# Performance work log

Measured on AMD Instinct MI355X. Metric: run time of the kernel, lower is better.

## Reference

```python
import jax, jax.numpy as jnp
import numpy as np

B, S, DIN, DOUT = 4, 2048, 4096, 4096
QMAX = 7  # int4 symmetric: values in [-8, 7]

def setup_inputs() -> dict:
    key = jax.random.key(0)
    kx, kq, ks, kb = jax.random.split(key, 4)
    x = jax.random.normal(kx, (B, S, DIN), dtype=jnp.float32)
    # int4 codes stored as int32, symmetric per-output-channel quantization
    qweight = jax.random.randint(kq, (DOUT, DIN), -8, 8, dtype=jnp.int32)
    # per-output-channel scale (max_abs / 7 style), strictly positive
    scale = jax.random.uniform(ks, (DOUT,), dtype=jnp.float32, minval=0.005, maxval=0.02)
    bias = jax.random.normal(kb, (DOUT,), dtype=jnp.float32)
    return {"x": x, "qweight": qweight, "scale": scale, "bias": bias}

def reference(x, qweight, scale, bias):
    # dequantize: per-output-channel scale broadcast over in_features
    weight = qweight.astype(jnp.float32) * scale[:, None]  # [DOUT, DIN]
    # F.linear: x @ weight.T + bias
    return jnp.einsum('bsi,oi->bso', x, weight) + bias
```

## Files before the change

### kernel.cpp

```cpp
#include <hip/hip_runtime.h>

typedef unsigned short u16;
typedef unsigned int u32;
typedef unsigned char u8;

typedef int i32x4 __attribute__((ext_vector_type(4)));

#define AS1 __attribute__((address_space(1)))
#define AS3 __attribute__((address_space(3)))

__global__ __launch_bounds__(256) void quant_x_kernel(
    const float* __restrict__ x, u8* __restrict__ xq, float* __restrict__ sx, int K)
{
    const int r = blockIdx.x;
    const int t = threadIdx.x;
    const float* xr = x + (size_t)r * K;
    float4 v[4];
    float m = 0.f;
#pragma unroll
    for (int i = 0; i < 4; ++i) {
        v[i] = *(const float4*)(xr + t * 16 + i * 4);
        m = fmaxf(m, fmaxf(fmaxf(fabsf(v[i].x), fabsf(v[i].y)),
                           fmaxf(fabsf(v[i].z), fabsf(v[i].w))));
    }
#pragma unroll
    for (int s = 32; s; s >>= 1) m = fmaxf(m, __shfl_xor(m, s));
    __shared__ float wm[4];
    if ((t & 63) == 0) wm[t >> 6] = m;
    __syncthreads();
    m = fmaxf(fmaxf(wm[0], wm[1]), fmaxf(wm[2], wm[3]));
    const float inv = 127.f / fmaxf(m, 1e-20f);
    if (t == 0) sx[r] = m * (1.f / 127.f);
    u32 o[4];
#pragma unroll
    for (int i = 0; i < 4; ++i) {
        int q0 = (int)rintf(v[i].x * inv), q1 = (int)rintf(v[i].y * inv);
        int q2 = (int)rintf(v[i].z * inv), q3 = (int)rintf(v[i].w * inv);
        o[i] = (u32)(q0 & 255) | ((u32)(q1 & 255) << 8) |
               ((u32)(q2 & 255) << 16) | ((u32)(q3 & 255) << 24);
    }
    *(uint4*)(xq + (size_t)r * K + t * 16) = make_uint4(o[0], o[1], o[2], o[3]);
}

__device__ __forceinline__ u32 pk8(int4 a) {
    return (u32)(a.x & 255) | ((u32)(a.y & 255) << 8) |
           ((u32)(a.z & 255) << 16) | ((u32)(a.w & 255) << 24);
}

__global__ void quant_w_kernel(const int4* __restrict__ q, uint4* __restrict__ y, int n16) {
    int stride = gridDim.x * blockDim.x;
    for (int i = blockIdx.x * blockDim.x + threadIdx.x; i < n16; i += stride) {
        int4 a = q[4 * i], b = q[4 * i + 1], c = q[4 * i + 2], d = q[4 * i + 3];
        y[i] = make_uint4(pk8(a), pk8(b), pk8(c), pk8(d));
    }
}


#define BM 256
#define BN 256
#define BKB 128

__global__ __launch_bounds__(256, 1) void gemm256_i8(
    const u8* __restrict__ A,
    const u8* __restrict__ W,
    const float* __restrict__ sx,
    const float* __restrict__ scale,
    const float* __restrict__ bias,
    float* __restrict__ C,
    int M, int N, int K)
{
    __shared__ alignas(1024) char lds[131072];

    const int nwg = gridDim.x;
    int bid = blockIdx.x;
    if ((nwg & 7) == 0) { int cpx = nwg >> 3; bid = (bid & 7) * cpx + (bid >> 3); }
    const int ntn = N / BN;
    const int tm = bid / ntn, tn = bid % ntn;

    const int t = threadIdx.x;
    const int l = t & 63;
    const int w = t >> 6;
    const int wm = w >> 1, wn = w & 1;
    const size_t Kz = (size_t)K;

    const int sRow = t >> 3;
    const int sCol = (((t & 7) ^ ((t >> 3) & 7)) * 16);
    const u8* aSrc = A + (size_t)(tm * BM + sRow) * Kz + sCol;
    const u8* bSrc = W + (size_t)(tn * BN + sRow) * Kz + sCol;
    const int wByte = w * 1024;

    char* dA0 = lds +      0 + wByte;
    char* dB0 = lds + 32768 + wByte;
    char* dA1 = lds + 65536 + wByte;
    char* dB1 = lds + 98304 + wByte;

    const int rowA = (wm * 128 + (l & 15)) * 128;
    const int rowB = (wn * 128 + (l & 15)) * 128;
    const int sl0 = (((l >> 4) | 0) ^ (l & 7)) * 16;
    const int sl1 = (((l >> 4) | 4) ^ (l & 7)) * 16;

    const char* aBase0 = lds +      0 + rowA;
    const char* bBase0 = lds + 32768 + rowB;
    const char* aBase1 = lds + 65536 + rowA;
    const char* bBase1 = lds + 98304 + rowB;

    i32x4 acc[8][8];
#pragma unroll
    for (int i = 0; i < 8; ++i)
#pragma unroll
        for (int j = 0; j < 8; ++j) acc[i][j] = (i32x4){0, 0, 0, 0};

    const int NT = K / BKB;

    auto stageTile = [&](char* dstA, char* dstB, int kt) {
#pragma unroll
        for (int c = 0; c < 8; ++c)
            __builtin_amdgcn_global_load_lds(
                (const AS1 void*)(aSrc + (size_t)c * 32 * Kz + (size_t)kt * BKB),
                (AS3 void*)(dstA + c * 4096), 16, 0, 0);
#pragma unroll
        for (int c = 0; c < 8; ++c)
            __builtin_amdgcn_global_load_lds(
                (const AS1 void*)(bSrc + (size_t)c * 32 * Kz + (size_t)kt * BKB),
                (AS3 void*)(dstB + c * 4096), 16, 0, 0);
    };
    auto readF = [&](i32x4 (&dst)[8], const char* base, int sl) {
#pragma unroll
        for (int f = 0; f < 8; ++f)
            dst[f] = *(const i32x4*)(base + f * 2048 + sl);
    };
    auto mfma64 = [&](i32x4 (&bf)[8], i32x4 (&af)[8]) {
#pragma unroll
        for (int f = 0; f < 8; ++f)
#pragma unroll
            for (int fn = 0; fn < 8; ++fn)
                acc[f][fn] = __builtin_amdgcn_mfma_i32_16x16x64_i8(
                    bf[fn], af[f], acc[f][fn], 0, 0, 0);
    };

#define SYNC_GATE  do { \
    asm volatile("s_waitcnt lgkmcnt(0)" ::: "memory"); \
    asm volatile("s_waitcnt vmcnt(0)"  ::: "memory"); \
    __builtin_amdgcn_s_barrier(); } while (0)

    stageTile(dA0, dB0, 0);
    stageTile(dA1, dB1, 1);
    asm volatile("s_waitcnt vmcnt(16)" ::: "memory");
    __builtin_amdgcn_s_barrier();

    i32x4 afrP[8], bfrP[8], afrQ[8], bfrQ[8];
    readF(afrP, aBase0, sl0);
    readF(bfrP, bBase0, sl0);

#pragma unroll 1
    for (int i = 0; i < NT / 2; ++i) {
        const int tE2 = (2 * i + 2) & (NT - 1);
        const int tO2 = (2 * i + 3) & (NT - 1);
        mfma64(bfrP, afrP);
        readF(afrQ, aBase0, sl1);
        readF(bfrQ, bBase0, sl1);
        SYNC_GATE;
        mfma64(bfrQ, afrQ);
        readF(afrP, aBase1, sl0);
        readF(bfrP, bBase1, sl0);
        stageTile(dA0, dB0, tE2);
        mfma64(bfrP, afrP);
        readF(afrQ, aBase1, sl1);
        readF(bfrQ, bBase1, sl1);
        SYNC_GATE;
        mfma64(bfrQ, afrQ);
        readF(afrP, aBase0, sl0);
        readF(bfrP, bBase0, sl0);
        stageTile(dA1, dB1, tO2);
    }

    const int mB = tm * BM + wm * 128 + (l & 15);
    const int nB = tn * BN + wn * 128 + 4 * (l >> 4);
    float sxv[8];
#pragma unroll
    for (int f = 0; f < 8; ++f) sxv[f] = sx[mB + f * 16];
#pragma unroll
    for (int fn = 0; fn < 8; ++fn) {
        const int n0 = nB + fn * 16;
        const float4 s4 = *(const float4*)(scale + n0);
        const float4 b4 = *(const float4*)(bias + n0);
#pragma unroll
        for (int f = 0; f < 8; ++f) {
            const int m = mB + f * 16;
            const float sm = sxv[f];
            float4 v;
            v.x = (float)acc[f][fn][0] * (sm * s4.x) + b4.x;
            v.y = (float)acc[f][fn][1] * (sm * s4.y) + b4.y;
            v.z = (float)acc[f][fn][2] * (sm * s4.z) + b4.z;
            v.w = (float)acc[f][fn][3] * (sm * s4.w) + b4.w;
            *(float4*)(C + (size_t)m * N + n0) = v;
        }
    }
#undef SYNC_GATE
}

extern "C" void kernel_launch(void* const* d_in, const int* in_sizes, int n_in,
                              void* d_out, int out_size, void* d_ws, size_t ws_size,
                              hipStream_t stream) {
    const float* x     = (const float*)d_in[0];
    const int*   qw    = (const int*)d_in[1];
    const float* scale = (const float*)d_in[2];
    const float* bias  = (const float*)d_in[3];
    float*       out   = (float*)d_out;

    const int N = in_sizes[2];
    const int K = in_sizes[1] / N;
    const int M = in_sizes[0] / K;

    u8*    xq = (u8*)d_ws;
    u8*    wq = xq + (size_t)M * K;
    float* sx = (float*)(wq + (size_t)N * K);

    quant_x_kernel<<<M, 256, 0, stream>>>(x, xq, sx, K);
    quant_w_kernel<<<2048, 256, 0, stream>>>((const int4*)qw, (uint4*)wq, (N * K) / 16);

    const int grid = (M / BM) * (N / BN);
    gemm256_i8<<<grid, 256, 0, stream>>>(xq, wq, sx, scale, bias, out, M, N, K);
}
```

Measured before the change: 217.6 us.

## Shrink GEMM tile to 128x128 with simple double-buffer loop and two blocks per CU

Replaces the 256x256 int8 GEMM tile (one workgroup per CU, 128KB LDS, hand-interleaved register ping-pong) with a 128x128 tile using 64KB LDS and launch bounds allowing two workgroups per CU. The main loop becomes a simple double-buffered pipeline: prefetch the next K tile, load all fragments, run MFMAs at raised priority, then wait and barrier. The intent is better occupancy and latency hiding across workgroups, plus four times as many blocks for load balance. In exchange, each tile reuses less data, so global/LDS traffic per MFMA doubles, and there is less intra-wave overlap of LDS reads with MFMA.

After: 200.3 us. 1.09x faster.

```diff
diff --git a/kernel.cpp b/kernel.cpp
--- a/kernel.cpp
+++ b/kernel.cpp
@@ -56,11 +56,11 @@
 }
 
 
-#define BM 256
-#define BN 256
+#define BM 128
+#define BN 128
 #define BKB 128
 
-__global__ __launch_bounds__(256, 1) void gemm256_i8(
+__global__ __launch_bounds__(256, 2) void gemm128_i8(
     const u8* __restrict__ A,
     const u8* __restrict__ W,
     const float* __restrict__ sx,
@@ -69,7 +69,7 @@
     float* __restrict__ C,
     int M, int N, int K)
 {
-    __shared__ alignas(1024) char lds[131072];
+    __shared__ alignas(1024) char lds[65536];
 
     const int nwg = gridDim.x;
     int bid = blockIdx.x;
@@ -89,103 +89,82 @@
     const u8* bSrc = W + (size_t)(tn * BN + sRow) * Kz + sCol;
     const int wByte = w * 1024;
 
-    char* dA0 = lds +      0 + wByte;
-    char* dB0 = lds + 32768 + wByte;
-    char* dA1 = lds + 65536 + wByte;
-    char* dB1 = lds + 98304 + wByte;
-
-    const int rowA = (wm * 128 + (l & 15)) * 128;
-    const int rowB = (wn * 128 + (l & 15)) * 128;
+    const int rowA = (wm * 64 + (l & 15)) * 128;
+    const int rowB = (wn * 64 + (l & 15)) * 128;
     const int sl0 = (((l >> 4) | 0) ^ (l & 7)) * 16;
     const int sl1 = (((l >> 4) | 4) ^ (l & 7)) * 16;
 
-    const char* aBase0 = lds +      0 + rowA;
-    const char* bBase0 = lds + 32768 + rowB;
-    const char* aBase1 = lds + 65536 + rowA;
-    const char* bBase1 = lds + 98304 + rowB;
-
-    i32x4 acc[8][8];
-#pragma unroll
-    for (int i = 0; i < 8; ++i)
-#pragma unroll
-        for (int j = 0; j < 8; ++j) acc[i][j] = (i32x4){0, 0, 0, 0};
+    i32x4 acc[4][4];
+#pragma unroll
+    for (int i = 0; i < 4; ++i)
+#pragma unroll
+        for (int j = 0; j < 4; ++j) acc[i][j] = (i32x4){0, 0, 0, 0};
 
     const int NT = K / BKB;
 
-    auto stageTile = [&](char* dstA, char* dstB, int kt) {
-#pragma unroll
-        for (int c = 0; c < 8; ++c)
+    auto stageTile = [&](int b, int kt) {
+        char* dA = lds + b * 32768 + wByte;
+        char* dB = lds + b * 32768 + 16384 + wByte;
+#pragma unroll
+        for (int c = 0; c < 4; ++c)
             __builtin_amdgcn_global_load_lds(
                 (const AS1 void*)(aSrc + (size_t)c * 32 * Kz + (size_t)kt * BKB),
-                (AS3 void*)(dstA + c * 4096), 16, 0, 0);
-#pragma unroll
-        for (int c = 0; c < 8; ++c)
+                (AS3 void*)(dA + c * 4096), 16, 0, 0);
+#pragma unroll
+        for (int c = 0; c < 4; ++c)
             __builtin_amdgcn_global_load_lds(
                 (const AS1 void*)(bSrc + (size_t)c * 32 * Kz + (size_t)kt * BKB),
-                (AS3 void*)(dstB + c * 4096), 16, 0, 0);
+                (AS3 void*)(dB + c * 4096), 16, 0, 0);
     };
-    auto readF = [&](i32x4 (&dst)[8], const char* base, int sl) {
-#pragma unroll
-        for (int f = 0; f < 8; ++f)
-            dst[f] = *(const i32x4*)(base + f * 2048 + sl);
-    };
-    auto mfma64 = [&](i32x4 (&bf)[8], i32x4 (&af)[8]) {
-#pragma unroll
-        for (int f = 0; f < 8; ++f)
-#pragma unroll
-            for (int fn = 0; fn < 8; ++fn)
-                acc[f][fn] = __builtin_amdgcn_mfma_i32_16x16x64_i8(
-                    bf[fn], af[f], acc[f][fn], 0, 0, 0);
-    };
-
-#define SYNC_GATE  do { \
-    asm volatile("s_waitcnt lgkmcnt(0)" ::: "memory"); \
-    asm volatile("s_waitcnt vmcnt(0)"  ::: "memory"); \
-    __builtin_amdgcn_s_barrier(); } while (0)
-
-    stageTile(dA0, dB0, 0);
-    stageTile(dA1, dB1, 1);
-    asm volatile("s_waitcnt vmcnt(16)" ::: "memory");
+
+    stageTile(0, 0);
+    asm volatile("s_waitcnt vmcnt(0)" ::: "memory");
     __builtin_amdgcn_s_barrier();
 
-    i32x4 afrP[8], bfrP[8], afrQ[8], bfrQ[8];
-    readF(afrP, aBase0, sl0);
-    readF(bfrP, bBase0, sl0);
-
 #pragma unroll 1
-    for (int i = 0; i < NT / 2; ++i) {
-        const int tE2 = (2 * i + 2) & (NT - 1);
-        const int tO2 = (2 * i + 3) & (NT - 1);
-        mfma64(bfrP, afrP);
-        readF(afrQ, aBase0, sl1);
-        readF(bfrQ, bBase0, sl1);
-        SYNC_GATE;
-        mfma64(bfrQ, afrQ);
-        readF(afrP, aBase1, sl0);
-        readF(bfrP, bBase1, sl0);
-        stageTile(dA0, dB0, tE2);
-        mfma64(bfrP, afrP);
-        readF(afrQ, aBase1, sl1);
-        readF(bfrQ, bBase1, sl1);
-        SYNC_GATE;
-        mfma64(bfrQ, afrQ);
-        readF(afrP, aBase0, sl0);
-        readF(bfrP, bBase0, sl0);
-        stageTile(dA1, dB1, tO2);
-    }
-
-    const int mB = tm * BM + wm * 128 + (l & 15);
-    const int nB = tn * BN + wn * 128 + 4 * (l >> 4);
-    float sxv[8];
-#pragma unroll
-    for (int f = 0; f < 8; ++f) sxv[f] = sx[mB + f * 16];
-#pragma unroll
-    for (int fn = 0; fn < 8; ++fn) {
+    for (int p = 0; p < NT; ++p) {
+        const int cur = p & 1;
+        stageTile(cur ^ 1, (p + 1) & (NT - 1));
+
+        const char* aB = lds + cur * 32768 + rowA;
+        const char* bB = lds + cur * 32768 + 16384 + rowB;
+        i32x4 aF[2][4], bF[2][4];
+#pragma unroll
+        for (int f = 0; f < 4; ++f) aF[0][f] = *(const i32x4*)(aB + f * 2048 + sl0);
+#pragma unroll
+        for (int f = 0; f < 4; ++f) bF[0][f] = *(const i32x4*)(bB + f * 2048 + sl0);
+#pragma unroll
+        for (int f = 0; f < 4; ++f) aF[1][f] = *(const i32x4*)(aB + f * 2048 + sl1);
+#pragma unroll
+        for (int f = 0; f < 4; ++f) bF[1][f] = *(const i32x4*)(bB + f * 2048 + sl1);
+
+        __builtin_amdgcn_s_setprio(1);
+#pragma unroll
+        for (int ks = 0; ks < 2; ++ks)
+#pragma unroll
+            for (int f = 0; f < 4; ++f)
+#pragma unroll
+                for (int fn = 0; fn < 4; ++fn)
+                    acc[f][fn] = __builtin_amdgcn_mfma_i32_16x16x64_i8(
+                        bF[ks][fn], aF[ks][f], acc[f][fn], 0, 0, 0);
+        __builtin_amdgcn_s_setprio(0);
+
+        asm volatile("s_waitcnt vmcnt(0) lgkmcnt(0)" ::: "memory");
+        __builtin_amdgcn_s_barrier();
+    }
+
+    const int mB = tm * BM + wm * 64 + (l & 15);
+    const int nB = tn * BN + wn * 64 + 4 * (l >> 4);
+    float sxv[4];
+#pragma unroll
+    for (int f = 0; f < 4; ++f) sxv[f] = sx[mB + f * 16];
+#pragma unroll
+    for (int fn = 0; fn < 4; ++fn) {
         const int n0 = nB + fn * 16;
         const float4 s4 = *(const float4*)(scale + n0);
         const float4 b4 = *(const float4*)(bias + n0);
 #pragma unroll
-        for (int f = 0; f < 8; ++f) {
+        for (int f = 0; f < 4; ++f) {
             const int m = mB + f * 16;
             const float sm = sxv[f];
             float4 v;
@@ -196,7 +175,6 @@
             *(float4*)(C + (size_t)m * N + n0) = v;
         }
     }
-#undef SYNC_GATE
 }
 
 extern "C" void kernel_launch(void* const* d_in, const int* in_sizes, int n_in,
@@ -220,5 +198,5 @@
     quant_w_kernel<<<2048, 256, 0, stream>>>((const int4*)qw, (uint4*)wq, (N * K) / 16);
 
     const int grid = (M / BM) * (N / BN);
-    gemm256_i8<<<grid, 256, 0, stream>>>(xq, wq, sx, scale, bias, out, M, N, K);
-}
+    gemm128_i8<<<grid, 256, 0, stream>>>(xq, wq, sx, scale, bias, out, M, N, K);
+}
```
